# Optimization experiments

Measured on AMD Instinct MI355X. Metric: run time of the kernel, lower is better.

Reference implementation:

```python
import math
import jax, jax.numpy as jnp
import numpy as np

B, Q, K, D = 32, 1024, 1024, 128
MASK_VALUE = -1000000.0


def setup_inputs() -> dict:
    key = jax.random.key(0)
    kq, kk, kv, kl = jax.random.split(key, 4)
    return {
        "queries": jax.random.normal(kq, (B, Q, D), dtype=jnp.float32),
        "keys": jax.random.normal(kk, (B, K, D), dtype=jnp.float32),
        "values": jax.random.normal(kv, (B, K, D), dtype=jnp.float32),
        "valid_lens": jax.random.randint(kl, (B,), 1, K + 1, dtype=jnp.int32),
    }


def reference(queries, keys, values, valid_lens):
    d = queries.shape[-1]
    # scores: [B, Q, K]
    scores = jnp.einsum("bqd,bkd->bqk", queries, keys) / math.sqrt(d)
    # key-padding mask: position k valid iff k < valid_lens[b] (broadcast over queries)
    mask = jnp.arange(keys.shape[1])[None, None, :] < valid_lens[:, None, None]
    scores = jnp.where(mask, scores, MASK_VALUE)
    attn = jax.nn.softmax(scores, axis=-1)
    # dropout p=0.0 -> identity
    return jnp.einsum("bqk,bkv->bqv", attn, values)
```

## Files before the change

### kernel.cpp

```cpp
#include <hip/hip_runtime.h>
#include <math.h>

typedef _Float16 f16;
typedef __attribute__((ext_vector_type(8))) _Float16 f16x8;
typedef __attribute__((ext_vector_type(4))) _Float16 f16x4;
typedef __attribute__((ext_vector_type(4))) float f32x4;

constexpr int BATCH = 32;
constexpr int QL = 1024;
constexpr int KL = 1024;
constexpr int D = 128;
constexpr int BQ = 128;
constexpr int BK = 64;
constexpr int CT = 8;
constexpr int DKP = 136;
constexpr int BKP = 72;

#define CSC 0.12752863187087177f

static __device__ __forceinline__ f16x4 pk4(float x, float y, float z, float w) {
  auto a = __builtin_amdgcn_cvt_pkrtz(x, y);
  auto b = __builtin_amdgcn_cvt_pkrtz(z, w);
  f16x4 h;
  h[0] = (f16)a[0]; h[1] = (f16)a[1]; h[2] = (f16)b[0]; h[3] = (f16)b[1];
  return h;
}
static __device__ __forceinline__ f16x8 pk8(float4 u, float4 v) {
  f16x4 a = pk4(u.x, u.y, u.z, u.w);
  f16x4 b = pk4(v.x, v.y, v.z, v.w);
  f16x8 h;
  h[0] = a[0]; h[1] = a[1]; h[2] = a[2]; h[3] = a[3];
  h[4] = b[0]; h[5] = b[1]; h[6] = b[2]; h[7] = b[3];
  return h;
}
static __device__ __forceinline__ f16x8 pk8v(f32x4 a, f32x4 b) {
  auto x0 = __builtin_amdgcn_cvt_pkrtz(a[0], a[1]);
  auto x1 = __builtin_amdgcn_cvt_pkrtz(a[2], a[3]);
  auto x2 = __builtin_amdgcn_cvt_pkrtz(b[0], b[1]);
  auto x3 = __builtin_amdgcn_cvt_pkrtz(b[2], b[3]);
  f16x8 h;
  h[0] = x0[0]; h[1] = x0[1]; h[2] = x1[0]; h[3] = x1[1];
  h[4] = x2[0]; h[5] = x2[1]; h[6] = x3[0]; h[7] = x3[1];
  return h;
}
static __device__ __forceinline__ f16x8 pk8s(float4 u, float4 v) {
  float4 a = {u.x * CSC, u.y * CSC, u.z * CSC, u.w * CSC};
  float4 b = {v.x * CSC, v.y * CSC, v.z * CSC, v.w * CSC};
  return pk8(a, b);
}

static __device__ __forceinline__ int krp(int kk) {
  return ((kk >> 5) << 5) | (((kk >> 2) & 1) << 4) | (((kk >> 3) & 3) << 2) | (kk & 3);
}

#define ISSUE(KR, VR, T)                                                   \
  do {                                                                     \
    const float4* Kt = (const float4*)(Kb + (size_t)(T) * BK * D);         \
    _Pragma("unroll")                                                      \
    for (int i_ = 0; i_ < 4; ++i_) {                                       \
      int cc_ = tid + i_ * 256;                                            \
      int row_ = cc_ >> 4, d04_ = (cc_ & 15) * 2;                          \
      KR[2 * i_]     = Kt[row_ * 32 + d04_];                               \
      KR[2 * i_ + 1] = Kt[row_ * 32 + d04_ + 1];                           \
    }                                                                      \
    const float* Vt = Vb + (size_t)(T) * BK * D;                           \
    _Pragma("unroll")                                                      \
    for (int i_ = 0; i_ < 2; ++i_) {                                       \
      int f_ = tid + i_ * 256;                                             \
      const float* base_ = Vt + (size_t)((f_ & 15) * 4) * D + (f_ >> 4) * 4; \
      VR[i_ * 4 + 0] = *(const float4*)(base_);                            \
      VR[i_ * 4 + 1] = *(const float4*)(base_ + D);                        \
      VR[i_ * 4 + 2] = *(const float4*)(base_ + 2 * D);                    \
      VR[i_ * 4 + 3] = *(const float4*)(base_ + 3 * D);                    \
    }                                                                      \
  } while (0)

#define DRAIN(KR, VR, NB)                                                  \
  do {                                                                     \
    _Pragma("unroll")                                                      \
    for (int i_ = 0; i_ < 4; ++i_) {                                       \
      int cc_ = tid + i_ * 256;                                            \
      int row_ = cc_ >> 4, d0_ = (cc_ & 15) * 8;                           \
      *(f16x8*)&sK[NB][krp(row_)][d0_] = pk8(KR[2 * i_], KR[2 * i_ + 1]);  \
    }                                                                      \
    _Pragma("unroll")                                                      \
    for (int i_ = 0; i_ < 2; ++i_) {                                       \
      int f_ = tid + i_ * 256;                                             \
      int k0_ = (f_ & 15) * 4, d0_ = (f_ >> 4) * 4;                        \
      float4 r0_ = VR[i_*4+0], r1_ = VR[i_*4+1], r2_ = VR[i_*4+2], r3_ = VR[i_*4+3]; \
      *(f16x4*)&sVT[NB][d0_ + 0][k0_] = pk4(r0_.x, r1_.x, r2_.x, r3_.x);   \
      *(f16x4*)&sVT[NB][d0_ + 1][k0_] = pk4(r0_.y, r1_.y, r2_.y, r3_.y);   \
      *(f16x4*)&sVT[NB][d0_ + 2][k0_] = pk4(r0_.z, r1_.z, r2_.z, r3_.z);   \
      *(f16x4*)&sVT[NB][d0_ + 3][k0_] = pk4(r0_.w, r1_.w, r2_.w, r3_.w);   \
    }                                                                      \
  } while (0)

#define TILE_BARRIER()                                                     \
  do {                                                                     \
    asm volatile("s_waitcnt lgkmcnt(0)" ::: "memory");                     \
    __builtin_amdgcn_s_barrier();                                          \
    asm volatile("" ::: "memory");                                         \
  } while (0)

__global__ __launch_bounds__(256, 2)
void attn_fwd(const float* __restrict__ Qp, const float* __restrict__ Kp,
              const float* __restrict__ Vp, const int* __restrict__ VLp,
              float* __restrict__ Op, float* __restrict__ wsO,
              float* __restrict__ wsL, int nks) {
  __shared__ f16 sK[2][BK][DKP];
  __shared__ f16 sVT[2][D][BKP];
  __shared__ int sN[32];
  __shared__ int sI[32];

  const int tid  = threadIdx.x;
  const int wave = tid >> 6, lane = tid & 63;
  const int l16  = lane & 15, quad = lane >> 4;

  if (tid < 32) sN[tid] = (VLp[tid] + BK - 1) / BK;
  __syncthreads();
  if (tid < 32) {
    int nb = sN[tid], r = 0;
    #pragma unroll
    for (int k = 0; k < 32; ++k) {
      int nk = sN[k];
      r += (nk > nb) || (nk == nb && k < tid);
    }
    sI[r] = tid;
  }
  __syncthreads();

  const int xcd = blockIdx.x & 7;
  const int i   = (int)blockIdx.x >> 3;

  int b, qt, ks, lb, t0, t1, nt, vl;
  if (nks == 2) {
    if (i < 32) { ks = 0; lb = i >> 3;              qt = i & 7; }
    else        { ks = 1; lb = 3 - ((i - 32) >> 3); qt = (i - 32) & 7; }
    const int gr = (lb == 0) ? xcd : (lb == 1) ? (15 - xcd)
                 : (lb == 2) ? (16 + xcd) : (31 - xcd);
    b  = sI[gr];
    vl = VLp[b];
    nt = (vl + BK - 1) / BK;
    t0 = ks * CT;
    t1 = min(nt, t0 + CT);
    if (t0 >= t1) return;
  } else {
    ks = 0; lb = i >> 3; qt = i & 7;
    const int gr = (lb == 0) ? xcd : (lb == 1) ? (15 - xcd)
                 : (lb == 2) ? (16 + xcd) : (31 - xcd);
    b  = sI[gr];
    vl = VLp[b];
    nt = (vl + BK - 1) / BK;
    t0 = 0; t1 = nt;
  }

  const float* Kb = Kp + (size_t)b * KL * D;
  const float* Vb = Vp + (size_t)b * KL * D;

  float4 kreg[8], vreg[8];

  const float* Qb = Qp + ((size_t)(b * QL + qt * BQ + wave * 32 + l16)) * D;
  float4 qtmp[16];
  #pragma unroll
  for (int h = 0; h < 2; ++h)
    #pragma unroll
    for (int kc = 0; kc < 4; ++kc) {
      const float* p = Qb + h * 16 * D + kc * 32 + quad * 8;
      qtmp[h * 8 + 2 * kc]     = *(const float4*)p;
      qtmp[h * 8 + 2 * kc + 1] = *(const float4*)(p + 4);
    }

  ISSUE(kreg, vreg, t0);

  f16x8 qf0[4], qf1[4];
  #pragma unroll
  for (int kc = 0; kc < 4; ++kc)
    qf0[kc] = pk8s(qtmp[2 * kc], qtmp[2 * kc + 1]);
  #pragma unroll
  for (int kc = 0; kc < 4; ++kc)
    qf1[kc] = pk8s(qtmp[8 + 2 * kc], qtmp[8 + 2 * kc + 1]);

  float ls0 = 0.f, ls1 = 0.f;
  f32x4 o0[8], o1[8];
  #pragma unroll
  for (int dt = 0; dt < 8; ++dt) {
    o0[dt] = (f32x4){0.f, 0.f, 0.f, 0.f};
    o1[dt] = (f32x4){0.f, 0.f, 0.f, 0.f};
  }

  DRAIN(kreg, vreg, 0);
  TILE_BARRIER();

  for (int t = t0; t < t1; ++t) {
    const int cur = (t - t0) & 1, nxt = cur ^ 1;
    const bool more = (t + 1 < t1);

    if (more) ISSUE(kreg, vreg, t + 1);

    f32x4 s0[4], s1[4];
    #pragma unroll
    for (int ct = 0; ct < 4; ++ct) {
      s0[ct] = (f32x4){0.f, 0.f, 0.f, 0.f};
      s1[ct] = (f32x4){0.f, 0.f, 0.f, 0.f};
      #pragma unroll
      for (int kc = 0; kc < 4; ++kc) {
        f16x8 kf = *(const f16x8*)&sK[cur][ct * 16 + l16][kc * 32 + quad * 8];
        s0[ct] = __builtin_amdgcn_mfma_f32_16x16x32_f16(kf, qf0[kc], s0[ct], 0, 0, 0);
        s1[ct] = __builtin_amdgcn_mfma_f32_16x16x32_f16(kf, qf1[kc], s1[ct], 0, 0, 0);
      }
    }

    if (t * BK + BK > vl) {
      #pragma unroll
      for (int ct = 0; ct < 4; ++ct) {
        int kb = t * BK + (ct >> 1) * 32 + (ct & 1) * 4 + quad * 8;
        #pragma unroll
        for (int r = 0; r < 4; ++r) {
          bool ok = (kb + r) < vl;
          s0[ct][r] = ok ? s0[ct][r] : -1.0e9f;
          s1[ct][r] = ok ? s1[ct][r] : -1.0e9f;
        }
      }
    }

    #pragma unroll
    for (int ct = 0; ct < 4; ++ct) {
      #pragma unroll
      for (int r = 0; r < 4; ++r) {
        float p0 = __builtin_amdgcn_exp2f(s0[ct][r]);
        float p1 = __builtin_amdgcn_exp2f(s1[ct][r]);
        s0[ct][r] = p0; ls0 += p0;
        s1[ct][r] = p1; ls1 += p1;
      }
    }
    f16x8 pa0 = pk8v(s0[0], s0[1]), pb0 = pk8v(s0[2], s0[3]);
    f16x8 pa1 = pk8v(s1[0], s1[1]), pb1 = pk8v(s1[2], s1[3]);

    #pragma unroll
    for (int dt = 0; dt < 8; ++dt) {
      f16x8 vf0 = *(const f16x8*)&sVT[cur][dt * 16 + l16][quad * 8];
      o0[dt] = __builtin_amdgcn_mfma_f32_16x16x32_f16(vf0, pa0, o0[dt], 0, 0, 0);
      o1[dt] = __builtin_amdgcn_mfma_f32_16x16x32_f16(vf0, pa1, o1[dt], 0, 0, 0);
      f16x8 vf1 = *(const f16x8*)&sVT[cur][dt * 16 + l16][32 + quad * 8];
      o0[dt] = __builtin_amdgcn_mfma_f32_16x16x32_f16(vf1, pb0, o0[dt], 0, 0, 0);
      o1[dt] = __builtin_amdgcn_mfma_f32_16x16x32_f16(vf1, pb1, o1[dt], 0, 0, 0);
    }

    if (more) DRAIN(kreg, vreg, nxt);
    TILE_BARRIER();
  }

  ls0 += __shfl_xor(ls0, 16);
  ls0 += __shfl_xor(ls0, 32);
  ls1 += __shfl_xor(ls1, 16);
  ls1 += __shfl_xor(ls1, 32);

  const int row0 = qt * BQ + wave * 32;
  if (nks == 1 || nt <= CT) {
    float* Ob = Op + ((size_t)(b * QL + row0)) * D;
    const float i0 = 1.0f / ls0, i1 = 1.0f / ls1;
    #pragma unroll
    for (int dt = 0; dt < 8; ++dt) {
      float4 w0 = {o0[dt][0] * i0, o0[dt][1] * i0, o0[dt][2] * i0, o0[dt][3] * i0};
      float4 w1 = {o1[dt][0] * i1, o1[dt][1] * i1, o1[dt][2] * i1, o1[dt][3] * i1};
      *(float4*)&Ob[(size_t)l16 * D + dt * 16 + quad * 4]        = w0;
      *(float4*)&Ob[(size_t)(16 + l16) * D + dt * 16 + quad * 4] = w1;
    }
  } else {
    const int pair = b * 8 + qt;
    float* dst = (ks == 0)
        ? Op + ((size_t)(b * QL + row0)) * D
        : wsO + (size_t)pair * BQ * D + (size_t)(wave * 32) * D;
    #pragma unroll
    for (int dt = 0; dt < 8; ++dt) {
      float4 w0 = {o0[dt][0], o0[dt][1], o0[dt][2], o0[dt][3]};
      float4 w1 = {o1[dt][0], o1[dt][1], o1[dt][2], o1[dt][3]};
      *(float4*)&dst[(size_t)l16 * D + dt * 16 + quad * 4]        = w0;
      *(float4*)&dst[(size_t)(16 + l16) * D + dt * 16 + quad * 4] = w1;
    }
    if (quad == 0) {
      wsL[(pair * 2 + ks) * 128 + wave * 32 + l16]      = ls0;
      wsL[(pair * 2 + ks) * 128 + wave * 32 + 16 + l16] = ls1;
    }
  }
}

__global__ __launch_bounds__(256)
void attn_combine(float* __restrict__ Op, const float* __restrict__ wsO,
                  const float* __restrict__ wsL, const int* __restrict__ VLp) {
  const int pair = blockIdx.x;
  const int b = pair >> 3;
  if (VLp[b] <= CT * BK) return;
  float* Ob = Op + ((size_t)(b * QL + (pair & 7) * BQ)) * D;
  const float4* o1 = (const float4*)(wsO + (size_t)pair * BQ * D);
  const float* Lt = wsL + (size_t)pair * 256;
  const int tid = threadIdx.x;
  #pragma unroll
  for (int i = 0; i < 16; ++i) {
    int fi = tid + i * 256;
    int row = fi >> 5;
    float inv = 1.0f / (Lt[row] + Lt[128 + row]);
    float4 a = ((const float4*)Ob)[fi];
    float4 c = o1[fi];
    float4 w = {(a.x + c.x) * inv, (a.y + c.y) * inv,
                (a.z + c.z) * inv, (a.w + c.w) * inv};
    ((float4*)Ob)[fi] = w;
  }
}

extern "C" void kernel_launch(void* const* d_in, const int* in_sizes, int n_in,
                              void* d_out, int out_size, void* d_ws, size_t ws_size,
                              hipStream_t stream) {
  const float* Qp = (const float*)d_in[0];
  const float* Kp = (const float*)d_in[1];
  const float* Vp = (const float*)d_in[2];
  const int*   VL = (const int*)d_in[3];
  float* Op = (float*)d_out;

  const size_t n_pairs = (size_t)BATCH * (QL / BQ);
  const size_t need = n_pairs * BQ * D * 4 + n_pairs * 256 * 4;
  if (d_ws != nullptr && ws_size >= need) {
    float* wsO = (float*)d_ws;
    float* wsL = (float*)d_ws + n_pairs * BQ * D;
    attn_fwd<<<dim3(2 * (int)n_pairs), dim3(256), 0, stream>>>(
        Qp, Kp, Vp, VL, Op, wsO, wsL, 2);
    attn_combine<<<dim3((int)n_pairs), dim3(256), 0, stream>>>(Op, wsO, wsL, VL);
  } else {
    attn_fwd<<<dim3((int)n_pairs), dim3(256), 0, stream>>>(
        Qp, Kp, Vp, VL, Op, nullptr, nullptr, 1);
  }
}
```

Before: 118.5 us.

## Fuse split-K combine into attention kernel via atomic last-arriver merge

Removes the separate combine kernel. Each split-K block writes its partial output and row sums, then bumps a per-tile atomic counter, and whichever block arrives second merges the other half with its own register accumulators and writes the normalized result. A memset is added to reset the counters every launch. The final-iteration barrier is also skipped when no next tile is pending. This trades a kernel launch and a reread of the partial output for a memset, fences and an atomic per block.

```diff
diff --git a/kernel.cpp b/kernel.cpp
--- a/kernel.cpp
+++ b/kernel.cpp
@@ -106,11 +106,12 @@
 void attn_fwd(const float* __restrict__ Qp, const float* __restrict__ Kp,
               const float* __restrict__ Vp, const int* __restrict__ VLp,
               float* __restrict__ Op, float* __restrict__ wsO,
-              float* __restrict__ wsL, int nks) {
+              float* __restrict__ wsL, int* __restrict__ wsC, int nks) {
   __shared__ f16 sK[2][BK][DKP];
   __shared__ f16 sVT[2][D][BKP];
   __shared__ int sN[32];
   __shared__ int sI[32];
+  __shared__ int sFlag;
 
   const int tid  = threadIdx.x;
   const int wave = tid >> 6, lane = tid & 63;
@@ -246,8 +247,10 @@
       o1[dt] = __builtin_amdgcn_mfma_f32_16x16x32_f16(vf1, pb1, o1[dt], 0, 0, 0);
     }
 
-    if (more) DRAIN(kreg, vreg, nxt);
-    TILE_BARRIER();
+    if (more) {
+      DRAIN(kreg, vreg, nxt);
+      TILE_BARRIER();
+    }
   }
 
   ls0 += __shfl_xor(ls0, 16);
@@ -282,29 +285,33 @@
       wsL[(pair * 2 + ks) * 128 + wave * 32 + l16]      = ls0;
       wsL[(pair * 2 + ks) * 128 + wave * 32 + 16 + l16] = ls1;
     }
-  }
-}
-
-__global__ __launch_bounds__(256)
-void attn_combine(float* __restrict__ Op, const float* __restrict__ wsO,
-                  const float* __restrict__ wsL, const int* __restrict__ VLp) {
-  const int pair = blockIdx.x;
-  const int b = pair >> 3;
-  if (VLp[b] <= CT * BK) return;
-  float* Ob = Op + ((size_t)(b * QL + (pair & 7) * BQ)) * D;
-  const float4* o1 = (const float4*)(wsO + (size_t)pair * BQ * D);
-  const float* Lt = wsL + (size_t)pair * 256;
-  const int tid = threadIdx.x;
-  #pragma unroll
-  for (int i = 0; i < 16; ++i) {
-    int fi = tid + i * 256;
-    int row = fi >> 5;
-    float inv = 1.0f / (Lt[row] + Lt[128 + row]);
-    float4 a = ((const float4*)Ob)[fi];
-    float4 c = o1[fi];
-    float4 w = {(a.x + c.x) * inv, (a.y + c.y) * inv,
-                (a.z + c.z) * inv, (a.w + c.w) * inv};
-    ((float4*)Ob)[fi] = w;
+
+    __threadfence();
+    __syncthreads();
+    if (tid == 0) sFlag = atomicAdd(&wsC[pair], 1);
+    __syncthreads();
+    if (sFlag == 1) {
+      __threadfence();
+      const int oks = ks ^ 1;
+      const float* osrc = (oks == 0)
+          ? Op + ((size_t)(b * QL + row0)) * D
+          : wsO + (size_t)pair * BQ * D + (size_t)(wave * 32) * D;
+      const float ol0 = wsL[(pair * 2 + oks) * 128 + wave * 32 + l16];
+      const float ol1 = wsL[(pair * 2 + oks) * 128 + wave * 32 + 16 + l16];
+      const float i0 = 1.0f / (ls0 + ol0), i1 = 1.0f / (ls1 + ol1);
+      float* Ob = Op + ((size_t)(b * QL + row0)) * D;
+      #pragma unroll
+      for (int dt = 0; dt < 8; ++dt) {
+        float4 c0 = *(const float4*)&osrc[(size_t)l16 * D + dt * 16 + quad * 4];
+        float4 c1 = *(const float4*)&osrc[(size_t)(16 + l16) * D + dt * 16 + quad * 4];
+        float4 w0 = {(o0[dt][0] + c0.x) * i0, (o0[dt][1] + c0.y) * i0,
+                     (o0[dt][2] + c0.z) * i0, (o0[dt][3] + c0.w) * i0};
+        float4 w1 = {(o1[dt][0] + c1.x) * i1, (o1[dt][1] + c1.y) * i1,
+                     (o1[dt][2] + c1.z) * i1, (o1[dt][3] + c1.w) * i1};
+        *(float4*)&Ob[(size_t)l16 * D + dt * 16 + quad * 4]        = w0;
+        *(float4*)&Ob[(size_t)(16 + l16) * D + dt * 16 + quad * 4] = w1;
+      }
+    }
   }
 }
 
@@ -318,15 +325,18 @@
   float* Op = (float*)d_out;
 
   const size_t n_pairs = (size_t)BATCH * (QL / BQ);
-  const size_t need = n_pairs * BQ * D * 4 + n_pairs * 256 * 4;
+  const size_t need = n_pairs * BQ * D * 4
+                    + n_pairs * 256 * 4
+                    + n_pairs * 4;
   if (d_ws != nullptr && ws_size >= need) {
     float* wsO = (float*)d_ws;
-    float* wsL = (float*)d_ws + n_pairs * BQ * D;
+    float* wsL = wsO + n_pairs * BQ * D;
+    int*   wsC = (int*)(wsL + n_pairs * 256);
+    hipMemsetAsync(wsC, 0, n_pairs * sizeof(int), stream);
     attn_fwd<<<dim3(2 * (int)n_pairs), dim3(256), 0, stream>>>(
-        Qp, Kp, Vp, VL, Op, wsO, wsL, 2);
-    attn_combine<<<dim3((int)n_pairs), dim3(256), 0, stream>>>(Op, wsO, wsL, VL);
+        Qp, Kp, Vp, VL, Op, wsO, wsL, wsC, 2);
   } else {
     attn_fwd<<<dim3((int)n_pairs), dim3(256), 0, stream>>>(
-        Qp, Kp, Vp, VL, Op, nullptr, nullptr, 1);
-  }
-}
+        Qp, Kp, Vp, VL, Op, nullptr, nullptr, nullptr, 1);
+  }
+}
```

After: 184.7 us. 55.8% more time.
